# Kernel tuning notes

Hardware: AMD Instinct MI355X
Metric: run time of the kernel (lower is better)

The kernel has to match this reference:

```python
import jax, jax.numpy as jnp
import numpy as np

N = 50000
E = 800000
F_IN = 128
HID = 64
G = 512
NEG_SLOPE = 0.2


def setup_inputs() -> dict:
    key = jax.random.key(0)
    ks = jax.random.split(key, 24)
    g = lambda i, shape: jax.random.normal(ks[i], shape, dtype=jnp.float32) * 0.1
    inp = {
        "x": jax.random.normal(ks[0], (N, F_IN), dtype=jnp.float32),
        "edge_index": jax.random.randint(ks[1], (2, E), 0, N),
        "edge_weight": jax.random.uniform(ks[2], (E, 1), dtype=jnp.float32),
        "batch": jnp.sort(jax.random.randint(ks[3], (N,), 0, G)),
        # layer 1
        "W1": g(4, (F_IN, HID)), "as1": g(5, (HID,)), "ad1": g(6, (HID,)),
        "We1": g(7, (1, HID)), "ae1": g(8, (HID,)), "b1": jnp.zeros((HID,), jnp.float32),
        # layer 2
        "W2": g(9, (HID, HID)), "as2": g(10, (HID,)), "ad2": g(11, (HID,)),
        "We2": g(12, (1, HID)), "ae2": g(13, (HID,)), "b2": jnp.zeros((HID,), jnp.float32),
        # layer 3
        "W3": g(14, (HID, HID)), "as3": g(15, (HID,)), "ad3": g(16, (HID,)),
        "We3": g(17, (1, HID)), "ae3": g(18, (HID,)), "b3": jnp.zeros((HID,), jnp.float32),
        # readout
        "lin_w": g(19, (HID, 1)), "lin_b": jnp.zeros((1,), jnp.float32),
    }
    return inp


def gat_layer(x, src, dst, eattr, W, att_s, att_d, We, att_e, bias):
    # x: [N,Fin]; src/dst: [Et]; eattr: [Et,1]
    h = x @ W                                  # [N,HID]
    a_src = h @ att_s                          # [N]
    a_dst = h @ att_d                          # [N]
    a_edge = (eattr @ We) @ att_e              # [Et]
    alpha = a_src[src] + a_dst[dst] + a_edge   # [Et]
    alpha = jax.nn.leaky_relu(alpha, NEG_SLOPE)
    # segment softmax over incoming edges of each dst node
    m = jax.ops.segment_max(alpha, dst, num_segments=N)
    alpha = jnp.exp(alpha - m[dst])
    s = jax.ops.segment_sum(alpha, dst, num_segments=N)
    alpha = alpha / (s[dst] + 1e-16)
    # weighted scatter-add of source features
    out = jax.ops.segment_sum(h[src] * alpha[:, None], dst, num_segments=N)
    return out + bias


def reference(x, edge_index, edge_weight, batch,
              W1, as1, ad1, We1, ae1, b1,
              W2, as2, ad2, We2, ae2, b2,
              W3, as3, ad3, We3, ae3, b3,
              lin_w, lin_b):
    # PyG GATConv default: add self-loops with edge_attr fill_value='mean'
    loop = jnp.arange(N)
    src = jnp.concatenate([edge_index[0], loop])
    dst = jnp.concatenate([edge_index[1], loop])
    mean_attr = jnp.mean(edge_weight, axis=0, keepdims=True)  # [1,1]
    eattr = jnp.concatenate([edge_weight, jnp.broadcast_to(mean_attr, (N, 1))], axis=0)

    h = gat_layer(x, src, dst, eattr, W1, as1, ad1, We1, ae1, b1)
    h = jax.nn.relu(h)
    h = gat_layer(h, src, dst, eattr, W2, as2, ad2, We2, ae2, b2)
    h = jax.nn.relu(h)
    h = gat_layer(h, src, dst, eattr, W3, as3, ad3, We3, ae3, b3)

    # global mean pool over graphs
    sums = jax.ops.segment_sum(h, batch, num_segments=G)          # [G,HID]
    counts = jax.ops.segment_sum(jnp.ones((N,), h.dtype), batch, num_segments=G)
    pooled = sums / jnp.maximum(counts, 1.0)[:, None]
    # dropout p=0.6 is identity at inference
    out = pooled @ lin_w + lin_b                                   # [G,1]
    return jax.nn.sigmoid(out)
```

## Files before the change

### kernel.cpp

```cpp
#include <hip/hip_runtime.h>
#include <math.h>

#define N_NODES 50000
#define N_EDGES 800000
#define F_IN_DIM 128
#define HID 64
#define NG 512
#define NEG 0.2f
#define SLICE ((N_NODES + 7) / 8)
#define EPB 2048
#define CAP 64
#define XGRID (((N_EDGES + EPB - 1) / EPB) * 8)
#define GGRID ((N_NODES + 63) / 64)

static __device__ __forceinline__ float wave_sum(float v) {
    for (int o = 32; o; o >>= 1) v += __shfl_xor(v, o, 64);
    return v;
}

static __device__ __forceinline__ unsigned short f2bf(float f) {
    union { float f; unsigned u; } v; v.f = f;
    unsigned r = (v.u + 0x7FFF + ((v.u >> 16) & 1)) >> 16;
    return (unsigned short)r;
}
static __device__ __forceinline__ float bf2f(unsigned short b) {
    union { unsigned u; float f; } v; v.u = ((unsigned)b) << 16;
    return v.f;
}

__global__ __launch_bounds__(256) void scatter_gemm1_k(
        const int* __restrict__ ei, const float* __restrict__ ew,
        int* __restrict__ deg, unsigned* __restrict__ bucket,
        uint2* __restrict__ ovf, int* __restrict__ ovf_cnt,
        float* __restrict__ mean_acc,
        const float* __restrict__ We1, const float* __restrict__ ae1,
        const float* __restrict__ We2, const float* __restrict__ ae2,
        const float* __restrict__ We3, const float* __restrict__ ae3,
        float* __restrict__ ce,
        const float* __restrict__ X, const float* __restrict__ W,
        const float* __restrict__ as_, const float* __restrict__ ad_,
        unsigned short* __restrict__ H, float* __restrict__ Asrc,
        float* __restrict__ Adst) {
    extern __shared__ float smem[];
    const int tid = threadIdx.x;

    if (blockIdx.x < XGRID) {
        int grp = blockIdx.x >> 3, slice = blockIdx.x & 7;
        int lo = slice * SLICE, hi = lo + SLICE;
        int base = grp * EPB;
        int off0 = base + (tid << 2);
        int off1 = off0 + 1024;
        const int* dstp = ei + N_EDGES;
        int4 d0 = make_int4(-1, -1, -1, -1), d1 = make_int4(-1, -1, -1, -1);
        if (off0 < N_EDGES) d0 = *(const int4*)(dstp + off0);
        if (off1 < N_EDGES) d1 = *(const int4*)(dstp + off1);

        float s = 0.f;
        if (slice == 0) {
            float4 w0 = {0, 0, 0, 0}, w1 = {0, 0, 0, 0};
            if (off0 < N_EDGES) w0 = *(const float4*)(ew + off0);
            if (off1 < N_EDGES) w1 = *(const float4*)(ew + off1);
            s = w0.x + w0.y + w0.z + w0.w + w1.x + w1.y + w1.z + w1.w;
        }

        const int dv[8] = {d0.x, d0.y, d0.z, d0.w, d1.x, d1.y, d1.z, d1.w};
        const int eo[8] = {off0, off0 + 1, off0 + 2, off0 + 3,
                           off1, off1 + 1, off1 + 2, off1 + 3};
        #pragma unroll
        for (int i = 0; i < 8; ++i) {
            int dst = dv[i];
            if (dst >= lo && dst < hi) {
                int e = eo[i];
                int src = ei[e];
                float w = ew[e];
                int pos = atomicAdd(&deg[dst], 1);
                unsigned entry = (unsigned)(src & 0xFFFF) | ((unsigned)f2bf(w) << 16);
                if (pos < CAP) bucket[(dst << 6) + pos] = entry;
                else { int op = atomicAdd(ovf_cnt, 1); ovf[op] = make_uint2((unsigned)dst, entry); }
            }
        }

        int lane = tid & 63, wv = tid >> 6;
        if (slice == 0) {
            s = wave_sum(s);
            if (lane == 0) smem[wv] = s;
            __syncthreads();
            if (tid == 0) atomicAdd(mean_acc, smem[0] + smem[1] + smem[2] + smem[3]);
        }
        if (blockIdx.x == 0 && wv >= 1) {
            const float* We = (wv == 1) ? We1 : (wv == 2) ? We2 : We3;
            const float* ae = (wv == 1) ? ae1 : (wv == 2) ? ae2 : ae3;
            float v = We[lane] * ae[lane];
            v = wave_sum(v);
            if (lane == 0) ce[wv - 1] = v;
        }
        return;
    }

    float* Xs = smem;
    float* Wt = smem + 64 * 17;
    const int tx = tid & 15, ty = tid >> 4;
    const int bid = blockIdx.x - XGRID;
    const int rowBase = bid * 64;

    float4 acc0 = {0,0,0,0}, acc1 = {0,0,0,0}, acc2 = {0,0,0,0}, acc3 = {0,0,0,0};
    const int xrow = tid >> 2;
    const int xkq  = tid & 3;
    const float4* W4 = (const float4*)W;
    float4* Wt4 = (float4*)Wt;

    #pragma unroll 2
    for (int kt = 0; kt < (F_IN_DIM >> 4); ++kt) {
        __syncthreads();
        int k0 = kt << 4;
        int grow = rowBase + xrow;
        float4 xv = {0,0,0,0};
        if (grow < N_NODES)
            xv = *(const float4*)(X + (size_t)grow * F_IN_DIM + k0 + (xkq << 2));
        float* xd = Xs + xrow * 17 + (xkq << 2);
        xd[0] = xv.x; xd[1] = xv.y; xd[2] = xv.z; xd[3] = xv.w;
        Wt4[tid] = W4[(kt << 8) + tid];
        __syncthreads();

        #pragma unroll
        for (int kk = 0; kk < 16; ++kk) {
            float4 b = *(const float4*)&Wt[kk * HID + (tx << 2)];
            float a0 = Xs[(ty * 4 + 0) * 17 + kk];
            float a1 = Xs[(ty * 4 + 1) * 17 + kk];
            float a2 = Xs[(ty * 4 + 2) * 17 + kk];
            float a3 = Xs[(ty * 4 + 3) * 17 + kk];
            acc0.x += a0 * b.x; acc0.y += a0 * b.y; acc0.z += a0 * b.z; acc0.w += a0 * b.w;
            acc1.x += a1 * b.x; acc1.y += a1 * b.y; acc1.z += a1 * b.z; acc1.w += a1 * b.w;
            acc2.x += a2 * b.x; acc2.y += a2 * b.y; acc2.z += a2 * b.z; acc2.w += a2 * b.w;
            acc3.x += a3 * b.x; acc3.y += a3 * b.y; acc3.z += a3 * b.z; acc3.w += a3 * b.w;
        }
    }

    float4 as4 = *(const float4*)(as_ + (tx << 2));
    float4 ad4 = *(const float4*)(ad_ + (tx << 2));
    float4 accs[4] = {acc0, acc1, acc2, acc3};
    #pragma unroll
    for (int i = 0; i < 4; ++i) {
        int row = rowBase + ty * 4 + i;
        if (row >= N_NODES) break;
        float4 a = accs[i];
        ushort4 hv;
        hv.x = f2bf(a.x); hv.y = f2bf(a.y); hv.z = f2bf(a.z); hv.w = f2bf(a.w);
        *(ushort4*)(H + (size_t)row * HID + (tx << 2)) = hv;
        float vs = a.x * as4.x + a.y * as4.y + a.z * as4.z + a.w * as4.w;
        float vd = a.x * ad4.x + a.y * ad4.y + a.z * ad4.z + a.w * ad4.w;
        #pragma unroll
        for (int o = 8; o; o >>= 1) { vs += __shfl_xor(vs, o, 64); vd += __shfl_xor(vd, o, 64); }
        if (tx == 0) { Asrc[row] = vs; Adst[row] = vd; }
    }
}

#define GATHA(sv0, sv1)                                                         \
    a0 = *(const ushort4*)(H + (size_t)(sv0).x * HID + (qlane << 2));           \
    a1 = *(const ushort4*)(H + (size_t)(sv0).y * HID + (qlane << 2));           \
    a2 = *(const ushort4*)(H + (size_t)(sv0).z * HID + (qlane << 2));           \
    a3 = *(const ushort4*)(H + (size_t)(sv0).w * HID + (qlane << 2));           \
    a4 = *(const ushort4*)(H + (size_t)(sv1).x * HID + (qlane << 2));           \
    a5 = *(const ushort4*)(H + (size_t)(sv1).y * HID + (qlane << 2));           \
    a6 = *(const ushort4*)(H + (size_t)(sv1).z * HID + (qlane << 2));           \
    a7 = *(const ushort4*)(H + (size_t)(sv1).w * HID + (qlane << 2));

#define GATHB(sv0, sv1)                                                         \
    b0 = *(const ushort4*)(H + (size_t)(sv0).x * HID + (qlane << 2));           \
    b1 = *(const ushort4*)(H + (size_t)(sv0).y * HID + (qlane << 2));           \
    b2 = *(const ushort4*)(H + (size_t)(sv0).z * HID + (qlane << 2));           \
    b3 = *(const ushort4*)(H + (size_t)(sv0).w * HID + (qlane << 2));           \
    b4 = *(const ushort4*)(H + (size_t)(sv1).x * HID + (qlane << 2));           \
    b5 = *(const ushort4*)(H + (size_t)(sv1).y * HID + (qlane << 2));           \
    b6 = *(const ushort4*)(H + (size_t)(sv1).z * HID + (qlane << 2));           \
    b7 = *(const ushort4*)(H + (size_t)(sv1).w * HID + (qlane << 2));

#define ACCA(pv0, pv1, ACC)                                                     \
    ACC.x += (pv0).x*bf2f(a0.x) + (pv0).y*bf2f(a1.x) + (pv0).z*bf2f(a2.x) + (pv0).w*bf2f(a3.x) \
           + (pv1).x*bf2f(a4.x) + (pv1).y*bf2f(a5.x) + (pv1).z*bf2f(a6.x) + (pv1).w*bf2f(a7.x); \
    ACC.y += (pv0).x*bf2f(a0.y) + (pv0).y*bf2f(a1.y) + (pv0).z*bf2f(a2.y) + (pv0).w*bf2f(a3.y) \
           + (pv1).x*bf2f(a4.y) + (pv1).y*bf2f(a5.y) + (pv1).z*bf2f(a6.y) + (pv1).w*bf2f(a7.y); \
    ACC.z += (pv0).x*bf2f(a0.z) + (pv0).y*bf2f(a1.z) + (pv0).z*bf2f(a2.z) + (pv0).w*bf2f(a3.z) \
           + (pv1).x*bf2f(a4.z) + (pv1).y*bf2f(a5.z) + (pv1).z*bf2f(a6.z) + (pv1).w*bf2f(a7.z); \
    ACC.w += (pv0).x*bf2f(a0.w) + (pv0).y*bf2f(a1.w) + (pv0).z*bf2f(a2.w) + (pv0).w*bf2f(a3.w) \
           + (pv1).x*bf2f(a4.w) + (pv1).y*bf2f(a5.w) + (pv1).z*bf2f(a6.w) + (pv1).w*bf2f(a7.w);

#define AGG_PHASE(ACC, DENOM)                                                   \
    {                                                                           \
        float a_self = Asrc[n] + ad + c * mv;                                   \
        a_self = (a_self > 0.f) ? a_self : NEG * a_self;                        \
        p_self = __expf(a_self);                                                \
        if (deg <= CAP) {                                                       \
            unsigned eent[4];                                                   \
            _Pragma("unroll")                                                   \
            for (int t = 0; t < 4; ++t) {                                       \
                int j = qlane + (t << 4);                                       \
                unsigned e = (j < deg) ? bucket[start + j] : 0u;                \
                eent[t] = e;                                                    \
                ls[slot][j] = (int)(e & 0xFFFF);                                \
            }                                                                   \
            __builtin_amdgcn_wave_barrier();                                    \
            int4 sA0 = *(int4*)&ls[slot][0];                                    \
            int4 sA1 = *(int4*)&ls[slot][4];                                    \
            ushort4 a0, a1, a2, a3, a4, a5, a6, a7;                             \
            ushort4 b0, b1, b2, b3, b4, b5, b6, b7;                             \
            GATHA(sA0, sA1)                              \
            rr = *(const ushort4*)(H + (size_t)n * HID + (qlane << 2));         \
            float lsum = 0.f;                                                   \
            _Pragma("unroll")                                                   \
            for (int t = 0; t < 4; ++t) {                                       \
                int j = qlane + (t << 4);                                       \
                float p = 0.f;                                                  \
                if (j < deg) {                                                  \
                    int s = (int)(eent[t] & 0xFFFF);                            \
                    float a = Asrc[s] + ad + c * bf2f((unsigned short)(eent[t] >> 16)); \
                    a = (a > 0.f) ? a : NEG * a;                                \
                    p = __expf(a);                                              \
                    lsum += p;                                                  \
                }                                                               \
                lp[slot][j] = p;                                                \
            }                                                                   \
            if (qlane == 0) lsum += p_self;                                     \
            _Pragma("unroll")                                                   \
            for (int o = 1; o < 16; o <<= 1) lsum += __shfl_xor(lsum, o, 64);   \
            DENOM = lsum;                                                       \
            __builtin_amdgcn_wave_barrier();                                    \
            int dpad = (deg + 7) & ~7;                                          \
            for (int j = 0; j < dpad; j += 8) {                                 \
                int jn = (j + 8 < dpad) ? j + 8 : j;                            \
                int4 t0 = *(int4*)&ls[slot][jn];                                \
                int4 t1 = *(int4*)&ls[slot][jn + 4];                            \
                GATHB(t0, t1)                         \
                float4 p0 = *(float4*)&lp[slot][j];                             \
                float4 p1 = *(float4*)&lp[slot][j + 4];                         \
                ACCA(p0, p1, ACC)                                               \
                a0 = b0; a1 = b1; a2 = b2; a3 = b3;                             \
                a4 = b4; a5 = b5; a6 = b6; a7 = b7;                             \
            }                                                                   \
        } else {                                                                \
            int novf = *ovf_cnt_p;                                              \
            float lsum = 0.f;                                                   \
            _Pragma("unroll")                                                   \
            for (int t = 0; t < 4; ++t) {                                       \
                int j = qlane + (t << 4);                                       \
                unsigned e = bucket[start + j];                                 \
                int s = e & 0xFFFF;                                             \
                float a = Asrc[s] + ad + c * bf2f((unsigned short)(e >> 16));   \
                a = (a > 0.f) ? a : NEG * a;                                    \
                float p = __expf(a);                                            \
                lsum += p;                                                      \
                lp[slot][j] = p;                                                \
                ls[slot][j] = s;                                                \
            }                                                                   \
            __builtin_amdgcn_wave_barrier();                                    \
            ushort4 a0, a1, a2, a3, a4, a5, a6, a7;                             \
            for (int j = 0; j < 64; j += 8) {                                   \
                float4 p0 = *(float4*)&lp[slot][j];                             \
                float4 p1 = *(float4*)&lp[slot][j + 4];                         \
                int4 s0 = *(int4*)&ls[slot][j];                                 \
                int4 s1 = *(int4*)&ls[slot][j + 4];                             \
                GATHA(s0, s1)                                                   \
                ACCA(p0, p1, ACC)                                               \
            }                                                                   \
            for (int i = 0; i < novf; ++i) {                                    \
                uint2 o = ovf[i];                                               \
                if ((int)o.x == n) {                                            \
                    unsigned e = o.y;                                           \
                    int s = e & 0xFFFF;                                         \
                    float a = Asrc[s] + ad + c * bf2f((unsigned short)(e >> 16));\
                    a = (a > 0.f) ? a : NEG * a;                                \
                    float p = __expf(a);                                        \
                    if (qlane == 0) lsum += p;                                  \
                    ushort4 r = *(const ushort4*)(H + (size_t)s * HID + (qlane << 2)); \
                    ACC.x += p * bf2f(r.x); ACC.y += p * bf2f(r.y);             \
                    ACC.z += p * bf2f(r.z); ACC.w += p * bf2f(r.w);             \
                }                                                               \
            }                                                                   \
            if (qlane == 0) lsum += p_self;                                     \
            _Pragma("unroll")                                                   \
            for (int o = 1; o < 16; o <<= 1) lsum += __shfl_xor(lsum, o, 64);   \
            DENOM = lsum;                                                       \
            rr = *(const ushort4*)(H + (size_t)n * HID + (qlane << 2));         \
        }                                                                       \
        ACC.x += p_self * bf2f(rr.x); ACC.y += p_self * bf2f(rr.y);             \
        ACC.z += p_self * bf2f(rr.z); ACC.w += p_self * bf2f(rr.w);             \
    }

__global__ __launch_bounds__(256) void agg_gemm_k(
        const unsigned short* __restrict__ H, const int* __restrict__ degArr,
        const unsigned* __restrict__ bucket,
        const uint2* __restrict__ ovf, const int* __restrict__ ovf_cnt_p,
        const float* __restrict__ Asrc, const float* __restrict__ Adst,
        const float* __restrict__ ceArr, int ci,
        const float* __restrict__ mean_acc,
        const float* __restrict__ bias,
        const float* __restrict__ Wn, const float* __restrict__ asn,
        const float* __restrict__ adn,
        unsigned short* __restrict__ H2, float* __restrict__ Asrc2,
        float* __restrict__ Adst2) {
    __shared__ float lp[16][64];
    __shared__ int   ls[16][64];
    __shared__ float Wl[64 * 64];
    __shared__ float rowBuf[16][68];
    const int tid = threadIdx.x;
    int wv = tid >> 6, lane = tid & 63;
    int qid = lane >> 4, qlane = lane & 15;
    int slot = wv * 4 + qid;
    int n = blockIdx.x * 16 + slot;

    {
        const float4* W4 = (const float4*)Wn;
        float4* Wl4 = (float4*)Wl;
        for (int i = tid; i < (HID * HID) >> 2; i += 256) Wl4[i] = W4[i];
    }

    int deg = degArr[n];
    int start = n << 6;
    float c = ceArr[ci];
    float ad = Adst[n];
    float mv = mean_acc[0] * (1.0f / (float)N_EDGES);
    float4 acc = {0, 0, 0, 0};
    float denom, p_self;
    ushort4 rr;

    AGG_PHASE(acc, denom)

    float inv = 1.f / (denom + 1e-16f);
    float4 b4 = *(const float4*)(bias + (qlane << 2));
    acc.x = fmaxf(acc.x * inv + b4.x, 0.f);
    acc.y = fmaxf(acc.y * inv + b4.y, 0.f);
    acc.z = fmaxf(acc.z * inv + b4.z, 0.f);
    acc.w = fmaxf(acc.w * inv + b4.w, 0.f);
    *(float4*)&rowBuf[slot][qlane << 2] = acc;
    __syncthreads();

    float4 h2 = {0, 0, 0, 0};
    #pragma unroll
    for (int k4 = 0; k4 < 16; ++k4) {
        float4 a4 = *(const float4*)&rowBuf[slot][k4 << 2];
        const float* wb = &Wl[(k4 << 2) * HID + (qlane << 2)];
        float4 w0 = *(const float4*)(wb);
        float4 w1 = *(const float4*)(wb + HID);
        float4 w2 = *(const float4*)(wb + 2 * HID);
        float4 w3 = *(const float4*)(wb + 3 * HID);
        h2.x += a4.x*w0.x + a4.y*w1.x + a4.z*w2.x + a4.w*w3.x;
        h2.y += a4.x*w0.y + a4.y*w1.y + a4.z*w2.y + a4.w*w3.y;
        h2.z += a4.x*w0.z + a4.y*w1.z + a4.z*w2.z + a4.w*w3.z;
        h2.w += a4.x*w0.w + a4.y*w1.w + a4.z*w2.w + a4.w*w3.w;
    }

    ushort4 hv;
    hv.x = f2bf(h2.x); hv.y = f2bf(h2.y); hv.z = f2bf(h2.z); hv.w = f2bf(h2.w);
    *(ushort4*)(H2 + (size_t)n * HID + (qlane << 2)) = hv;

    float4 as4 = *(const float4*)(asn + (qlane << 2));
    float4 ad4 = *(const float4*)(adn + (qlane << 2));
    float vs = h2.x * as4.x + h2.y * as4.y + h2.z * as4.z + h2.w * as4.w;
    float vd = h2.x * ad4.x + h2.y * ad4.y + h2.z * ad4.z + h2.w * ad4.w;
    #pragma unroll
    for (int o = 8; o; o >>= 1) { vs += __shfl_xor(vs, o, 64); vd += __shfl_xor(vd, o, 64); }
    if (qlane == 0) { Asrc2[n] = vs; Adst2[n] = vd; }
}

__global__ __launch_bounds__(256) void aggregate_k(
        const unsigned short* __restrict__ H, const int* __restrict__ degArr,
        const unsigned* __restrict__ bucket,
        const uint2* __restrict__ ovf, const int* __restrict__ ovf_cnt_p,
        const float* __restrict__ Asrc, const float* __restrict__ Adst,
        const float* __restrict__ ceArr, int ci,
        const float* __restrict__ mean_acc,
        const float* __restrict__ bias, float* __restrict__ Out) {
    __shared__ float lp[16][64];
    __shared__ int   ls[16][64];
    int wv = threadIdx.x >> 6, lane = threadIdx.x & 63;
    int qid = lane >> 4, qlane = lane & 15;
    int slot = wv * 4 + qid;
    int n = blockIdx.x * 16 + slot;
    if (n >= N_NODES) return;
    int deg = degArr[n];
    int start = n << 6;
    float c = ceArr[ci];
    float ad = Adst[n];
    float mv = mean_acc[0] * (1.0f / (float)N_EDGES);
    float4 acc = {0, 0, 0, 0};
    float denom, p_self;
    ushort4 rr;

    AGG_PHASE(acc, denom)

    float inv = 1.f / (denom + 1e-16f);
    float4 b4 = *(const float4*)(bias + (qlane << 2));
    acc.x = acc.x * inv + b4.x;
    acc.y = acc.y * inv + b4.y;
    acc.z = acc.z * inv + b4.z;
    acc.w = acc.w * inv + b4.w;
    *(float4*)(Out + (size_t)n * HID + (qlane << 2)) = acc;
}

__global__ __launch_bounds__(256) void pool_readout_k(
        const float* __restrict__ act, const int* __restrict__ batch,
        const float* __restrict__ lin_w, const float* __restrict__ lin_b,
        float* __restrict__ out) {
    int wv = threadIdx.x >> 6, lane = threadIdx.x & 63;
    int g = blockIdx.x * 4 + wv;
    if (g >= NG) return;
    int lo = 0, hi = N_NODES;
    while (lo < hi) { int m = (lo + hi) >> 1; if (batch[m] < g) lo = m + 1; else hi = m; }
    int start = lo;
    hi = N_NODES;
    while (lo < hi) { int m = (lo + hi) >> 1; if (batch[m] < g + 1) lo = m + 1; else hi = m; }
    int end = lo;
    float acc = 0.f;
    int n = start;
    for (; n + 4 <= end; n += 4) {
        float v0 = act[(size_t)n * HID + lane];
        float v1 = act[(size_t)(n + 1) * HID + lane];
        float v2 = act[(size_t)(n + 2) * HID + lane];
        float v3 = act[(size_t)(n + 3) * HID + lane];
        acc += v0 + v1 + v2 + v3;
    }
    for (; n < end; ++n) acc += act[(size_t)n * HID + lane];
    float cntf = (float)(end - start);
    float v = acc / fmaxf(cntf, 1.f) * lin_w[lane];
    v = wave_sum(v);
    if (lane == 0) {
        float z = v + lin_b[0];
        out[g] = 1.f / (1.f + __expf(-z));
    }
}

extern "C" void kernel_launch(void* const* d_in, const int* in_sizes, int n_in,
                              void* d_out, int out_size, void* d_ws, size_t ws_size,
                              hipStream_t stream) {
    const float* x     = (const float*)d_in[0];
    const int*   ei    = (const int*)d_in[1];
    const float* ew    = (const float*)d_in[2];
    const int*   batch = (const int*)d_in[3];
    const float* W1  = (const float*)d_in[4];
    const float* as1 = (const float*)d_in[5];
    const float* ad1 = (const float*)d_in[6];
    const float* We1 = (const float*)d_in[7];
    const float* ae1 = (const float*)d_in[8];
    const float* b1  = (const float*)d_in[9];
    const float* W2  = (const float*)d_in[10];
    const float* as2 = (const float*)d_in[11];
    const float* ad2 = (const float*)d_in[12];
    const float* We2 = (const float*)d_in[13];
    const float* ae2 = (const float*)d_in[14];
    const float* b2  = (const float*)d_in[15];
    const float* W3  = (const float*)d_in[16];
    const float* as3 = (const float*)d_in[17];
    const float* ad3 = (const float*)d_in[18];
    const float* We3 = (const float*)d_in[19];
    const float* ae3 = (const float*)d_in[20];
    const float* b3  = (const float*)d_in[21];
    const float* lin_w = (const float*)d_in[22];
    const float* lin_b = (const float*)d_in[23];
    float* out = (float*)d_out;

    char* w = (char*)d_ws;
    size_t off = 0;
    auto alloc = [&](size_t bytes) -> void* {
        void* p = w + off;
        off = (off + bytes + 255) & ~(size_t)255;
        return p;
    };
    int*   deg      = (int*)alloc(N_NODES * sizeof(int));
    float* mean_acc = (float*)alloc(sizeof(float));
    int*   ovf_cnt  = (int*)alloc(sizeof(int));
    size_t zero_bytes = off;
    float* ce      = (float*)alloc(4 * sizeof(float));
    unsigned* bucket = (unsigned*)alloc((size_t)N_NODES * CAP * sizeof(unsigned));
    uint2* ovf     = (uint2*)alloc((size_t)N_EDGES * sizeof(uint2));
    float* a_src   = (float*)alloc(N_NODES * sizeof(float));
    float* a_dst   = (float*)alloc(N_NODES * sizeof(float));
    float* a_src2  = (float*)alloc(N_NODES * sizeof(float));
    float* a_dst2  = (float*)alloc(N_NODES * sizeof(float));
    unsigned short* hbuf  = (unsigned short*)alloc((size_t)N_NODES * HID * sizeof(unsigned short));
    unsigned short* hbuf2 = (unsigned short*)alloc((size_t)N_NODES * HID * sizeof(unsigned short));
    float* actA    = (float*)alloc((size_t)N_NODES * HID * sizeof(float));

    hipMemsetAsync(d_ws, 0, zero_bytes, stream);

    int agrid = (N_NODES + 15) / 16;
    size_t lds_f = (size_t)(64 * 17 + 16 * 64) * sizeof(float);

    scatter_gemm1_k<<<XGRID + GGRID, 256, lds_f, stream>>>(
        ei, ew, deg, bucket, ovf, ovf_cnt, mean_acc,
        We1, ae1, We2, ae2, We3, ae3, ce,
        x, W1, as1, ad1, hbuf, a_src, a_dst);

    agg_gemm_k<<<agrid, 256, 0, stream>>>(hbuf, deg, bucket, ovf, ovf_cnt,
                                          a_src, a_dst, ce, 0, mean_acc, b1,
                                          W2, as2, ad2, hbuf2, a_src2, a_dst2);

    agg_gemm_k<<<agrid, 256, 0, stream>>>(hbuf2, deg, bucket, ovf, ovf_cnt,
                                          a_src2, a_dst2, ce, 1, mean_acc, b2,
                                          W3, as3, ad3, hbuf, a_src, a_dst);

    aggregate_k<<<agrid, 256, 0, stream>>>(hbuf, deg, bucket, ovf, ovf_cnt,
                                           a_src, a_dst, ce, 2, mean_acc, b3, actA);

    pool_readout_k<<<NG / 4, 256, 0, stream>>>(actA, batch, lin_w, lin_b, out);
}
```

Baseline: 266.2 us.

## Replicate bf16 feature table 8x so each XCD gathers from a private copy

```diff
diff --git a/kernel.cpp b/kernel.cpp
--- a/kernel.cpp
+++ b/kernel.cpp
@@ -12,6 +12,7 @@
 #define CAP 64
 #define XGRID (((N_EDGES + EPB - 1) / EPB) * 8)
 #define GGRID ((N_NODES + 63) / 64)
+#define HCPY ((size_t)N_NODES * HID)
 
 static __device__ __forceinline__ float wave_sum(float v) {
     for (int o = 32; o; o >>= 1) v += __shfl_xor(v, o, 64);
@@ -146,7 +147,9 @@
         float4 a = accs[i];
         ushort4 hv;
         hv.x = f2bf(a.x); hv.y = f2bf(a.y); hv.z = f2bf(a.z); hv.w = f2bf(a.w);
-        *(ushort4*)(H + (size_t)row * HID + (tx << 2)) = hv;
+        #pragma unroll
+        for (int cp = 0; cp < 8; ++cp)
+            *(ushort4*)(H + cp * HCPY + (size_t)row * HID + (tx << 2)) = hv;
         float vs = a.x * as4.x + a.y * as4.y + a.z * as4.z + a.w * as4.w;
         float vd = a.x * ad4.x + a.y * ad4.y + a.z * ad4.z + a.w * ad4.w;
         #pragma unroll
@@ -156,24 +159,24 @@
 }
 
 #define GATHA(sv0, sv1)                                                         \
-    a0 = *(const ushort4*)(H + (size_t)(sv0).x * HID + (qlane << 2));           \
-    a1 = *(const ushort4*)(H + (size_t)(sv0).y * HID + (qlane << 2));           \
-    a2 = *(const ushort4*)(H + (size_t)(sv0).z * HID + (qlane << 2));           \
-    a3 = *(const ushort4*)(H + (size_t)(sv0).w * HID + (qlane << 2));           \
-    a4 = *(const ushort4*)(H + (size_t)(sv1).x * HID + (qlane << 2));           \
-    a5 = *(const ushort4*)(H + (size_t)(sv1).y * HID + (qlane << 2));           \
-    a6 = *(const ushort4*)(H + (size_t)(sv1).z * HID + (qlane << 2));           \
-    a7 = *(const ushort4*)(H + (size_t)(sv1).w * HID + (qlane << 2));
+    a0 = *(const ushort4*)(Hl + (size_t)(sv0).x * HID + (qlane << 2));          \
+    a1 = *(const ushort4*)(Hl + (size_t)(sv0).y * HID + (qlane << 2));          \
+    a2 = *(const ushort4*)(Hl + (size_t)(sv0).z * HID + (qlane << 2));          \
+    a3 = *(const ushort4*)(Hl + (size_t)(sv0).w * HID + (qlane << 2));          \
+    a4 = *(const ushort4*)(Hl + (size_t)(sv1).x * HID + (qlane << 2));          \
+    a5 = *(const ushort4*)(Hl + (size_t)(sv1).y * HID + (qlane << 2));          \
+    a6 = *(const ushort4*)(Hl + (size_t)(sv1).z * HID + (qlane << 2));          \
+    a7 = *(const ushort4*)(Hl + (size_t)(sv1).w * HID + (qlane << 2));
 
 #define GATHB(sv0, sv1)                                                         \
-    b0 = *(const ushort4*)(H + (size_t)(sv0).x * HID + (qlane << 2));           \
-    b1 = *(const ushort4*)(H + (size_t)(sv0).y * HID + (qlane << 2));           \
-    b2 = *(const ushort4*)(H + (size_t)(sv0).z * HID + (qlane << 2));           \
-    b3 = *(const ushort4*)(H + (size_t)(sv0).w * HID + (qlane << 2));           \
-    b4 = *(const ushort4*)(H + (size_t)(sv1).x * HID + (qlane << 2));           \
-    b5 = *(const ushort4*)(H + (size_t)(sv1).y * HID + (qlane << 2));           \
-    b6 = *(const ushort4*)(H + (size_t)(sv1).z * HID + (qlane << 2));           \
-    b7 = *(const ushort4*)(H + (size_t)(sv1).w * HID + (qlane << 2));
+    b0 = *(const ushort4*)(Hl + (size_t)(sv0).x * HID + (qlane << 2));          \
+    b1 = *(const ushort4*)(Hl + (size_t)(sv0).y * HID + (qlane << 2));          \
+    b2 = *(const ushort4*)(Hl + (size_t)(sv0).z * HID + (qlane << 2));          \
+    b3 = *(const ushort4*)(Hl + (size_t)(sv0).w * HID + (qlane << 2));          \
+    b4 = *(const ushort4*)(Hl + (size_t)(sv1).x * HID + (qlane << 2));          \
+    b5 = *(const ushort4*)(Hl + (size_t)(sv1).y * HID + (qlane << 2));          \
+    b6 = *(const ushort4*)(Hl + (size_t)(sv1).z * HID + (qlane << 2));          \
+    b7 = *(const ushort4*)(Hl + (size_t)(sv1).w * HID + (qlane << 2));
 
 #define ACCA(pv0, pv1, ACC)                                                     \
     ACC.x += (pv0).x*bf2f(a0.x) + (pv0).y*bf2f(a1.x) + (pv0).z*bf2f(a2.x) + (pv0).w*bf2f(a3.x) \
@@ -205,7 +208,7 @@
             ushort4 a0, a1, a2, a3, a4, a5, a6, a7;                             \
             ushort4 b0, b1, b2, b3, b4, b5, b6, b7;                             \
             GATHA(sA0, sA1)                              \
-            rr = *(const ushort4*)(H + (size_t)n * HID + (qlane << 2));         \
+            rr = *(const ushort4*)(Hl + (size_t)n * HID + (qlane << 2));        \
             float lsum = 0.f;                                                   \
             _Pragma("unroll")                                                   \
             for (int t = 0; t < 4; ++t) {                                       \
@@ -271,7 +274,7 @@
                     a = (a > 0.f) ? a : NEG * a;                                \
                     float p = __expf(a);                                        \
                     if (qlane == 0) lsum += p;                                  \
-                    ushort4 r = *(const ushort4*)(H + (size_t)s * HID + (qlane << 2)); \
+                    ushort4 r = *(const ushort4*)(Hl + (size_t)s * HID + (qlane << 2)); \
                     ACC.x += p * bf2f(r.x); ACC.y += p * bf2f(r.y);             \
                     ACC.z += p * bf2f(r.z); ACC.w += p * bf2f(r.w);             \
                 }                                                               \
@@ -280,7 +283,7 @@
             _Pragma("unroll")                                                   \
             for (int o = 1; o < 16; o <<= 1) lsum += __shfl_xor(lsum, o, 64);   \
             DENOM = lsum;                                                       \
-            rr = *(const ushort4*)(H + (size_t)n * HID + (qlane << 2));         \
+            rr = *(const ushort4*)(Hl + (size_t)n * HID + (qlane << 2));        \
         }                                                                       \
         ACC.x += p_self * bf2f(rr.x); ACC.y += p_self * bf2f(rr.y);             \
         ACC.z += p_self * bf2f(rr.z); ACC.w += p_self * bf2f(rr.w);             \
@@ -307,6 +310,7 @@
     int qid = lane >> 4, qlane = lane & 15;
     int slot = wv * 4 + qid;
     int n = blockIdx.x * 16 + slot;
+    const unsigned short* Hl = H + (size_t)(blockIdx.x & 7) * HCPY;
 
     {
         const float4* W4 = (const float4*)Wn;
@@ -351,7 +355,9 @@
 
     ushort4 hv;
     hv.x = f2bf(h2.x); hv.y = f2bf(h2.y); hv.z = f2bf(h2.z); hv.w = f2bf(h2.w);
-    *(ushort4*)(H2 + (size_t)n * HID + (qlane << 2)) = hv;
+    #pragma unroll
+    for (int cp = 0; cp < 8; ++cp)
+        *(ushort4*)(H2 + cp * HCPY + (size_t)n * HID + (qlane << 2)) = hv;
 
     float4 as4 = *(const float4*)(asn + (qlane << 2));
     float4 ad4 = *(const float4*)(adn + (qlane << 2));
@@ -377,6 +383,7 @@
     int slot = wv * 4 + qid;
     int n = blockIdx.x * 16 + slot;
     if (n >= N_NODES) return;
+    const unsigned short* Hl = H + (size_t)(blockIdx.x & 7) * HCPY;
     int deg = degArr[n];
     int start = n << 6;
     float c = ceArr[ci];
@@ -476,8 +483,8 @@
     float* a_dst   = (float*)alloc(N_NODES * sizeof(float));
     float* a_src2  = (float*)alloc(N_NODES * sizeof(float));
     float* a_dst2  = (float*)alloc(N_NODES * sizeof(float));
-    unsigned short* hbuf  = (unsigned short*)alloc((size_t)N_NODES * HID * sizeof(unsigned short));
-    unsigned short* hbuf2 = (unsigned short*)alloc((size_t)N_NODES * HID * sizeof(unsigned short));
+    unsigned short* hbuf  = (unsigned short*)alloc(8 * HCPY * sizeof(unsigned short));
+    unsigned short* hbuf2 = (unsigned short*)alloc(8 * HCPY * sizeof(unsigned short));
     float* actA    = (float*)alloc((size_t)N_NODES * HID * sizeof(float));
 
     hipMemsetAsync(d_ws, 0, zero_bytes, stream);
```

Result: slower. 275.7 us (+3.6%).

## Project final-layer features onto readout weights before mean pooling

Applied to the files above, without the earlier changes.

```diff
diff --git a/kernel.cpp b/kernel.cpp
--- a/kernel.cpp
+++ b/kernel.cpp
@@ -362,14 +362,15 @@
     if (qlane == 0) { Asrc2[n] = vs; Adst2[n] = vd; }
 }
 
-__global__ __launch_bounds__(256) void aggregate_k(
+__global__ __launch_bounds__(256) void aggregate_scalar_k(
         const unsigned short* __restrict__ H, const int* __restrict__ degArr,
         const unsigned* __restrict__ bucket,
         const uint2* __restrict__ ovf, const int* __restrict__ ovf_cnt_p,
         const float* __restrict__ Asrc, const float* __restrict__ Adst,
         const float* __restrict__ ceArr, int ci,
         const float* __restrict__ mean_acc,
-        const float* __restrict__ bias, float* __restrict__ Out) {
+        const float* __restrict__ bias, const float* __restrict__ lin_w,
+        float* __restrict__ Sout) {
     __shared__ float lp[16][64];
     __shared__ int   ls[16][64];
     int wv = threadIdx.x >> 6, lane = threadIdx.x & 63;
@@ -390,17 +391,19 @@
 
     float inv = 1.f / (denom + 1e-16f);
     float4 b4 = *(const float4*)(bias + (qlane << 2));
-    acc.x = acc.x * inv + b4.x;
-    acc.y = acc.y * inv + b4.y;
-    acc.z = acc.z * inv + b4.z;
-    acc.w = acc.w * inv + b4.w;
-    *(float4*)(Out + (size_t)n * HID + (qlane << 2)) = acc;
+    float4 lw = *(const float4*)(lin_w + (qlane << 2));
+    float s = (acc.x * inv + b4.x) * lw.x
+            + (acc.y * inv + b4.y) * lw.y
+            + (acc.z * inv + b4.z) * lw.z
+            + (acc.w * inv + b4.w) * lw.w;
+    #pragma unroll
+    for (int o = 8; o; o >>= 1) s += __shfl_xor(s, o, 64);
+    if (qlane == 0) Sout[n] = s;
 }
 
 __global__ __launch_bounds__(256) void pool_readout_k(
-        const float* __restrict__ act, const int* __restrict__ batch,
-        const float* __restrict__ lin_w, const float* __restrict__ lin_b,
-        float* __restrict__ out) {
+        const float* __restrict__ S, const int* __restrict__ batch,
+        const float* __restrict__ lin_b, float* __restrict__ out) {
     int wv = threadIdx.x >> 6, lane = threadIdx.x & 63;
     int g = blockIdx.x * 4 + wv;
     if (g >= NG) return;
@@ -411,20 +414,11 @@
     while (lo < hi) { int m = (lo + hi) >> 1; if (batch[m] < g + 1) lo = m + 1; else hi = m; }
     int end = lo;
     float acc = 0.f;
-    int n = start;
-    for (; n + 4 <= end; n += 4) {
-        float v0 = act[(size_t)n * HID + lane];
-        float v1 = act[(size_t)(n + 1) * HID + lane];
-        float v2 = act[(size_t)(n + 2) * HID + lane];
-        float v3 = act[(size_t)(n + 3) * HID + lane];
-        acc += v0 + v1 + v2 + v3;
-    }
-    for (; n < end; ++n) acc += act[(size_t)n * HID + lane];
-    float cntf = (float)(end - start);
-    float v = acc / fmaxf(cntf, 1.f) * lin_w[lane];
-    v = wave_sum(v);
+    for (int n = start + lane; n < end; n += 64) acc += S[n];
+    acc = wave_sum(acc);
     if (lane == 0) {
-        float z = v + lin_b[0];
+        float cntf = (float)(end - start);
+        float z = acc / fmaxf(cntf, 1.f) + lin_b[0];
         out[g] = 1.f / (1.f + __expf(-z));
     }
 }
@@ -478,7 +472,7 @@
     float* a_dst2  = (float*)alloc(N_NODES * sizeof(float));
     unsigned short* hbuf  = (unsigned short*)alloc((size_t)N_NODES * HID * sizeof(unsigned short));
     unsigned short* hbuf2 = (unsigned short*)alloc((size_t)N_NODES * HID * sizeof(unsigned short));
-    float* actA    = (float*)alloc((size_t)N_NODES * HID * sizeof(float));
+    float* Sbuf    = (float*)alloc(N_NODES * sizeof(float));
 
     hipMemsetAsync(d_ws, 0, zero_bytes, stream);
 
@@ -498,8 +492,9 @@
                                           a_src2, a_dst2, ce, 1, mean_acc, b2,
                                           W3, as3, ad3, hbuf, a_src, a_dst);
 
-    aggregate_k<<<agrid, 256, 0, stream>>>(hbuf, deg, bucket, ovf, ovf_cnt,
-                                           a_src, a_dst, ce, 2, mean_acc, b3, actA);
-
-    pool_readout_k<<<NG / 4, 256, 0, stream>>>(actA, batch, lin_w, lin_b, out);
-}
+    aggregate_scalar_k<<<agrid, 256, 0, stream>>>(hbuf, deg, bucket, ovf, ovf_cnt,
+                                                  a_src, a_dst, ce, 2, mean_acc,
+                                                  b3, lin_w, Sbuf);
+
+    pool_readout_k<<<NG / 4, 256, 0, stream>>>(Sbuf, batch, lin_b, out);
+}
```

New measurement: 262.8 us. No clear change (-1.3%).
